# Kernel optimization log

Hardware: AMD Instinct MI355X
Metric: run time of the kernel (lower is better)

The kernel has to match this reference:

```python
import jax, jax.numpy as jnp
import numpy as np
import math

NUM_IN_C = 128      # rep_2d num_c (c_z)
ATT_C = 64          # attention_num_c
NUM_HEADS = 4
B, T, I, J = 1, 4, 256, 256


def setup_inputs() -> dict:
    key = jax.random.key(0)
    ks = jax.random.split(key, 7)
    s = 1.0 / math.sqrt(NUM_IN_C)
    return {
        "z2d": jax.random.normal(ks[0], (B, I, J, NUM_IN_C), dtype=jnp.float32),
        "t2d": jax.random.normal(ks[1], (B, T, I, J, NUM_IN_C), dtype=jnp.float32),
        # nn.Linear weights are [out_features, in_features]; apply as x @ W.T
        "Wq": jax.random.normal(ks[2], (ATT_C * NUM_HEADS, NUM_IN_C), dtype=jnp.float32) * s,
        "Wk": jax.random.normal(ks[3], (ATT_C * NUM_HEADS, NUM_IN_C), dtype=jnp.float32) * s,
        "Wv": jax.random.normal(ks[4], (ATT_C * NUM_HEADS, NUM_IN_C), dtype=jnp.float32) * s,
        "Wo": jax.random.normal(ks[5], (NUM_IN_C, ATT_C * NUM_HEADS), dtype=jnp.float32) * s,
        "bo": jax.random.normal(ks[6], (NUM_IN_C,), dtype=jnp.float32) * 0.02,
    }


def reference(z2d, t2d, Wq, Wk, Wv, Wo, bo):
    # Projections; reshape last dim to (attention_num_c, num_heads) per torch .view
    q = (z2d @ Wq.T).reshape(*z2d.shape[:-1], ATT_C, NUM_HEADS)        # b i j c h
    k = (t2d @ Wk.T).reshape(*t2d.shape[:-1], ATT_C, NUM_HEADS)        # b t i j c h
    v = (t2d @ Wv.T).reshape(*t2d.shape[:-1], ATT_C, NUM_HEADS)        # b t i j c h
    # NOTE: original scales by sqrt(num_in_c), not sqrt(attention_num_c)
    scores = jnp.einsum('bijch,btijch->btijh', q, k) / math.sqrt(NUM_IN_C)
    w = jax.nn.softmax(scores, axis=1)                                  # softmax over template axis t
    out = jnp.einsum('btijh,btijch->bijch', w, v)                       # b i j c h
    out = out.reshape(*out.shape[:-2], ATT_C * NUM_HEADS)               # flatten (c,h)
    return out @ Wo.T + bo
```

## Files before the change

### kernel.cpp

```cpp
#include <hip/hip_runtime.h>


#define PIX 65536

typedef __attribute__((ext_vector_type(8))) short s8v;
typedef __attribute__((ext_vector_type(4))) float f4v;
typedef __attribute__((ext_vector_type(4))) unsigned int u4v;
typedef __attribute__((ext_vector_type(4))) float fl4;

__device__ __forceinline__ unsigned short f2bf(float x) {
    unsigned int u = __float_as_uint(x);
    u = (u + 0x7FFFu + ((u >> 16) & 1u)) >> 16;
    return (unsigned short)u;
}
__device__ __forceinline__ float bf2fs(short v) {
    return __uint_as_float(((unsigned int)(unsigned short)v) << 16);
}

__device__ __forceinline__ unsigned int cvtpk(float lo, float hi) {
    unsigned int r;
    asm("v_cvt_pk_bf16_f32 %0, %1, %2" : "=v"(r) : "v"(lo), "v"(hi));
    return r;
}

__device__ __forceinline__ s8v pack8(fl4 d0, fl4 d1) {
    union { u4v u; s8v s; } cv;
    cv.u[0] = cvtpk(d0[0], d0[1]);
    cv.u[1] = cvtpk(d0[2], d0[3]);
    cv.u[2] = cvtpk(d1[0], d1[1]);
    cv.u[3] = cvtpk(d1[2], d1[3]);
    return cv.s;
}

__device__ __forceinline__ float bflo(unsigned int u) { return __uint_as_float(u << 16); }
__device__ __forceinline__ float bfhi(unsigned int u) { return __uint_as_float(u & 0xffff0000u); }

__global__ __launch_bounds__(256) void build_weights(
        const float* __restrict__ Wq, const float* __restrict__ Wk,
        const float* __restrict__ Wv, const float* __restrict__ Wo,
        unsigned short* __restrict__ mcat, unsigned short* __restrict__ pcat) {
    int b = blockIdx.x;
    if (b < 256) {
        int idx = b * 256 + threadIdx.x;
        int n = idx >> 7, k1 = idx & 127;
        int h = n >> 7, k2 = n & 127;
        float s = 0.f;
        #pragma unroll 8
        for (int c = 0; c < 64; c++) {
            int r = c * 4 + h;
            s += Wq[r * 128 + k1] * Wk[r * 128 + k2];
        }
        mcat[idx] = f2bf(s * 0.088388347648318447f);
    } else {
        int idx = (b - 256) * 256 + threadIdx.x;
        int m = idx >> 9, kk = idx & 511;
        int h = kk >> 7, k = kk & 127;
        float s = 0.f;
        #pragma unroll 8
        for (int c = 0; c < 64; c++) {
            int r = c * 4 + h;
            s += Wo[m * 256 + r] * Wv[r * 128 + k];
        }
        pcat[idx] = f2bf(s);
    }
}

#define S_USH (512 * 136)

__global__ __launch_bounds__(512, 2) void score_kernel(
    const float* __restrict__ z2d, const float* __restrict__ t2d,
    const unsigned short* __restrict__ mcat, float* __restrict__ wbuf) {

    __shared__ unsigned short sm[S_USH];
    const int tid = threadIdx.x;

    #pragma unroll
    for (int i = 0; i < 16; i++) {
        int g8 = i * 512 + tid;
        int row = g8 >> 4, c8 = g8 & 15;
        *(u4v*)&sm[row * 136 + c8 * 8] = *(const u4v*)(mcat + (size_t)g8 * 8);
    }
    __syncthreads();

    const int wv = tid >> 6, lane = tid & 63, quad = lane >> 4, l15 = lane & 15;

    for (int it = 0; it < 2; it++) {
        const int p = blockIdx.x * 256 + (wv * 2 + it) * 16 + l15;

        s8v za[4];
        {
            const float* zp = z2d + (size_t)p * 128 + quad * 8;
            #pragma unroll
            for (int ks = 0; ks < 4; ks++)
                za[ks] = pack8(*(const fl4*)(zp + ks * 32), *(const fl4*)(zp + ks * 32 + 4));
        }

        float ps[4][4];
        #pragma unroll
        for (int h = 0; h < 4; h++)
            #pragma unroll
            for (int t = 0; t < 4; t++) ps[h][t] = 0.f;

        const float* apb = t2d + (size_t)p * 128 + quad * 4;

        #pragma unroll 2
        for (int cb = 0; cb < 8; cb++) {
            unsigned int a2[4][2];
            #pragma unroll
            for (int t = 0; t < 4; t++) {
                const fl4 v = *(const fl4*)(apb + (size_t)t * (PIX * 128) + cb * 16);
                a2[t][0] = cvtpk(v[0], v[1]);
                a2[t][1] = cvtpk(v[2], v[3]);
            }
            #pragma unroll
            for (int h = 0; h < 4; h++) {
                f4v u = {0.f, 0.f, 0.f, 0.f};
                #pragma unroll
                for (int ks = 0; ks < 4; ks++) {
                    const s8v a = *(const s8v*)&sm[(h * 128 + cb * 16 + l15) * 136 +
                                                   ks * 32 + quad * 8];
                    u = __builtin_amdgcn_mfma_f32_16x16x32_bf16(a, za[ks], u, 0, 0, 0);
                }
                #pragma unroll
                for (int t = 0; t < 4; t++) {
                    ps[h][t] += u[0] * bflo(a2[t][0]) + u[1] * bfhi(a2[t][0])
                              + u[2] * bflo(a2[t][1]) + u[3] * bfhi(a2[t][1]);
                }
            }
        }

        #pragma unroll
        for (int h = 0; h < 4; h++) {
            float s0 = ps[h][0], s1 = ps[h][1], s2 = ps[h][2], s3 = ps[h][3];
            s0 += __shfl_xor(s0, 16); s0 += __shfl_xor(s0, 32);
            s1 += __shfl_xor(s1, 16); s1 += __shfl_xor(s1, 32);
            s2 += __shfl_xor(s2, 16); s2 += __shfl_xor(s2, 32);
            s3 += __shfl_xor(s3, 16); s3 += __shfl_xor(s3, 32);
            const float mx = fmaxf(fmaxf(s0, s1), fmaxf(s2, s3));
            const float e0 = __expf(s0 - mx), e1 = __expf(s1 - mx);
            const float e2 = __expf(s2 - mx), e3 = __expf(s3 - mx);
            const float inv = 1.f / (e0 + e1 + e2 + e3);
            if (quad == 0) {
                float* wp = wbuf + (size_t)h * 4 * PIX + p;
                wp[0 * PIX] = e0 * inv; wp[1 * PIX] = e1 * inv;
                wp[2 * PIX] = e2 * inv; wp[3 * PIX] = e3 * inv;
            }
        }
    }
}

#define O_USH (128 * 520)

__global__ __launch_bounds__(512, 2) void out_kernel(
    const float* __restrict__ t2d, const unsigned short* __restrict__ pcat,
    const float* __restrict__ wbuf, const float* __restrict__ bo,
    float* __restrict__ out) {

    __shared__ unsigned short sm[O_USH];
    const int tid = threadIdx.x;

    #pragma unroll
    for (int i = 0; i < 16; i++) {
        int g8 = i * 512 + tid;
        int row = g8 >> 6, c8 = g8 & 63;
        *(u4v*)&sm[row * 520 + c8 * 8] = *(const u4v*)(pcat + (size_t)g8 * 8);
    }
    __syncthreads();

    const int wv = tid >> 6, lane = tid & 63, quad = lane >> 4, l15 = lane & 15;
    const int p0 = blockIdx.x * 256 + wv * 32;

    float wgt[4][2][4];
    #pragma unroll
    for (int h = 0; h < 4; h++)
        #pragma unroll
        for (int t = 0; t < 4; t++)
            #pragma unroll
            for (int mt = 0; mt < 2; mt++)
                wgt[t][mt][h] = wbuf[(size_t)(h * 4 + t) * PIX + p0 + mt * 16 + l15];

    f4v acc[2][8];
    #pragma unroll
    for (int mt = 0; mt < 2; mt++)
        #pragma unroll
        for (int ct = 0; ct < 8; ct++) acc[mt][ct] = (f4v){0.f, 0.f, 0.f, 0.f};

    #pragma unroll
    for (int ks = 0; ks < 4; ks++) {
        s8v ab[4][2];
        #pragma unroll
        for (int t = 0; t < 4; t++)
            #pragma unroll
            for (int mt = 0; mt < 2; mt++) {
                const float* ap = t2d + ((size_t)t * PIX + p0 + mt * 16 + l15) * 128
                                  + ks * 32 + quad * 8;
                const fl4 d0 = *(const fl4*)ap;
                const fl4 d1 = *(const fl4*)(ap + 4);
                s8v a;
                a[0] = (short)f2bf(d0[0]); a[1] = (short)f2bf(d0[1]);
                a[2] = (short)f2bf(d0[2]); a[3] = (short)f2bf(d0[3]);
                a[4] = (short)f2bf(d1[0]); a[5] = (short)f2bf(d1[1]);
                a[6] = (short)f2bf(d1[2]); a[7] = (short)f2bf(d1[3]);
                ab[t][mt] = a;
            }
        #pragma unroll
        for (int h = 0; h < 4; h++) {
            s8v af[2];
            #pragma unroll
            for (int mt = 0; mt < 2; mt++) {
                s8v o;
                #pragma unroll
                for (int j = 0; j < 8; j++) {
                    float v = wgt[0][mt][h] * bf2fs(ab[0][mt][j])
                            + wgt[1][mt][h] * bf2fs(ab[1][mt][j])
                            + wgt[2][mt][h] * bf2fs(ab[2][mt][j])
                            + wgt[3][mt][h] * bf2fs(ab[3][mt][j]);
                    o[j] = (short)f2bf(v);
                }
                af[mt] = o;
            }
            #pragma unroll
            for (int ct = 0; ct < 8; ct++) {
                const s8v b = *(const s8v*)&sm[(ct * 16 + l15) * 520
                                               + h * 128 + ks * 32 + quad * 8];
                acc[0][ct] = __builtin_amdgcn_mfma_f32_16x16x32_bf16(af[0], b, acc[0][ct], 0, 0, 0);
                acc[1][ct] = __builtin_amdgcn_mfma_f32_16x16x32_bf16(af[1], b, acc[1][ct], 0, 0, 0);
            }
        }
    }

    #pragma unroll
    for (int ct = 0; ct < 8; ct++) {
        const float bb = bo[ct * 16 + l15];
        #pragma unroll
        for (int mt = 0; mt < 2; mt++)
            #pragma unroll
            for (int r = 0; r < 4; r++)
                out[(size_t)(p0 + mt * 16 + quad * 4 + r) * 128 + ct * 16 + l15]
                    = acc[mt][ct][r] + bb;
    }
}

extern "C" void kernel_launch(void* const* d_in, const int* in_sizes, int n_in,
                              void* d_out, int out_size, void* d_ws, size_t ws_size,
                              hipStream_t stream) {
    const float* z2d = (const float*)d_in[0];
    const float* t2d = (const float*)d_in[1];
    const float* Wq  = (const float*)d_in[2];
    const float* Wk  = (const float*)d_in[3];
    const float* Wv  = (const float*)d_in[4];
    const float* Wo  = (const float*)d_in[5];
    const float* bo  = (const float*)d_in[6];

    unsigned short* mcat = (unsigned short*)d_ws;
    unsigned short* pcat = mcat + 512 * 128;
    float* wbuf = (float*)(pcat + 128 * 512);

    build_weights<<<512, 256, 0, stream>>>(Wq, Wk, Wv, Wo, mcat, pcat);
    score_kernel<<<256, 512, 0, stream>>>(z2d, t2d, mcat, wbuf);
    out_kernel<<<256, 512, 0, stream>>>(t2d, pcat, wbuf, bo, (float*)d_out);
}
```

Measured before the change: 277.5 us.

## Double-buffer t2d loads in score kernel and drop bf16 rounding of keys

Restructures the score kernel's channel loop into a software pipeline. Two register buffers of t2d fp32 values are prefetched ahead of the MFMA compute, and the z2d loads are hoisted before the conversion. The loaded t2d values are now used directly in fp32 instead of being packed to bf16 and unpacked, which removes the conversion instructions and slightly changes numerics. The aim is to hide global load latency behind MFMA work, at the cost of higher register pressure under the 512-thread, 2-block launch bounds.

```diff
diff --git a/kernel.cpp b/kernel.cpp
--- a/kernel.cpp
+++ b/kernel.cpp
@@ -31,9 +31,6 @@
     cv.u[3] = cvtpk(d1[2], d1[3]);
     return cv.s;
 }
-
-__device__ __forceinline__ float bflo(unsigned int u) { return __uint_as_float(u << 16); }
-__device__ __forceinline__ float bfhi(unsigned int u) { return __uint_as_float(u & 0xffff0000u); }
 
 __global__ __launch_bounds__(256) void build_weights(
         const float* __restrict__ Wq, const float* __restrict__ Wk,
@@ -67,6 +64,35 @@
 
 #define S_USH (512 * 136)
 
+#define LOADP(dst, cb2) do {                                                   \
+    _Pragma("unroll")                                                          \
+    for (int t = 0; t < 4; t++) {                                              \
+        dst[t * 2]     = *(const fl4*)(apb + (size_t)t * (PIX * 128) + (cb2) * 16);      \
+        dst[t * 2 + 1] = *(const fl4*)(apb + (size_t)t * (PIX * 128) + (cb2) * 16 + 16); \
+    } } while (0)
+
+#define COMPP(src, cb2) do {                                                   \
+    _Pragma("unroll")                                                          \
+    for (int uu = 0; uu < 2; uu++) {                                           \
+        const int rowb = (((cb2) + uu) * 16 + l15) * 136 + quad * 8;           \
+        _Pragma("unroll")                                                      \
+        for (int h = 0; h < 4; h++) {                                          \
+            f4v uacc = {0.f, 0.f, 0.f, 0.f};                                   \
+            _Pragma("unroll")                                                  \
+            for (int ks = 0; ks < 4; ks++) {                                   \
+                const s8v a = *(const s8v*)&sm[h * (128 * 136) + rowb + ks * 32]; \
+                uacc = __builtin_amdgcn_mfma_f32_16x16x32_bf16(a, za[ks], uacc, 0, 0, 0); \
+            }                                                                  \
+            _Pragma("unroll")                                                  \
+            for (int t = 0; t < 4; t++) {                                      \
+                ps[h][t] += uacc[0] * src[t * 2 + uu][0]                       \
+                          + uacc[1] * src[t * 2 + uu][1]                       \
+                          + uacc[2] * src[t * 2 + uu][2]                       \
+                          + uacc[3] * src[t * 2 + uu][3];                      \
+            }                                                                  \
+        }                                                                      \
+    } } while (0)
+
 __global__ __launch_bounds__(512, 2) void score_kernel(
     const float* __restrict__ z2d, const float* __restrict__ t2d,
     const unsigned short* __restrict__ mcat, float* __restrict__ wbuf) {
@@ -84,16 +110,27 @@
 
     const int wv = tid >> 6, lane = tid & 63, quad = lane >> 4, l15 = lane & 15;
 
+    #pragma unroll 1
     for (int it = 0; it < 2; it++) {
         const int p = blockIdx.x * 256 + (wv * 2 + it) * 16 + l15;
+        const float* zp  = z2d + (size_t)p * 128 + quad * 8;
+        const float* apb = t2d + (size_t)p * 128 + quad * 4;
+
+        fl4 zr[8];
+        #pragma unroll
+        for (int ks = 0; ks < 4; ks++) {
+            zr[ks * 2]     = *(const fl4*)(zp + ks * 32);
+            zr[ks * 2 + 1] = *(const fl4*)(zp + ks * 32 + 4);
+        }
+
+        fl4 pA[8], pB[8];
+        LOADP(pA, 0);
+        LOADP(pB, 2);
 
         s8v za[4];
-        {
-            const float* zp = z2d + (size_t)p * 128 + quad * 8;
-            #pragma unroll
-            for (int ks = 0; ks < 4; ks++)
-                za[ks] = pack8(*(const fl4*)(zp + ks * 32), *(const fl4*)(zp + ks * 32 + 4));
-        }
+        #pragma unroll
+        for (int ks = 0; ks < 4; ks++)
+            za[ks] = pack8(zr[ks * 2], zr[ks * 2 + 1]);
 
         float ps[4][4];
         #pragma unroll
@@ -101,33 +138,12 @@
             #pragma unroll
             for (int t = 0; t < 4; t++) ps[h][t] = 0.f;
 
-        const float* apb = t2d + (size_t)p * 128 + quad * 4;
-
-        #pragma unroll 2
-        for (int cb = 0; cb < 8; cb++) {
-            unsigned int a2[4][2];
-            #pragma unroll
-            for (int t = 0; t < 4; t++) {
-                const fl4 v = *(const fl4*)(apb + (size_t)t * (PIX * 128) + cb * 16);
-                a2[t][0] = cvtpk(v[0], v[1]);
-                a2[t][1] = cvtpk(v[2], v[3]);
-            }
-            #pragma unroll
-            for (int h = 0; h < 4; h++) {
-                f4v u = {0.f, 0.f, 0.f, 0.f};
-                #pragma unroll
-                for (int ks = 0; ks < 4; ks++) {
-                    const s8v a = *(const s8v*)&sm[(h * 128 + cb * 16 + l15) * 136 +
-                                                   ks * 32 + quad * 8];
-                    u = __builtin_amdgcn_mfma_f32_16x16x32_bf16(a, za[ks], u, 0, 0, 0);
-                }
-                #pragma unroll
-                for (int t = 0; t < 4; t++) {
-                    ps[h][t] += u[0] * bflo(a2[t][0]) + u[1] * bfhi(a2[t][0])
-                              + u[2] * bflo(a2[t][1]) + u[3] * bfhi(a2[t][1]);
-                }
-            }
-        }
+        COMPP(pA, 0);
+        LOADP(pA, 4);
+        COMPP(pB, 2);
+        LOADP(pB, 6);
+        COMPP(pA, 4);
+        COMPP(pB, 6);
 
         #pragma unroll
         for (int h = 0; h < 4; h++) {
```

Result: no change. 278.2 us (+0.3%).
